# Kernel optimization log

Measured on AMD Instinct MI355X. Metric: run time of the kernel, lower is better.

Reference implementation:

```python
import jax, jax.numpy as jnp
import numpy as np

HIDDEN = 512
N_HEAD = 8
D_HEAD = 64
MAX_REL = 3
B, S = 2, 2048


def setup_inputs() -> dict:
    key = jax.random.key(0)
    ks = jax.random.split(key, 12)
    sc = 1.0 / np.sqrt(HIDDEN)
    return {
        "query": jax.random.normal(ks[0], (B, S, HIDDEN), jnp.float32),
        "key_": jax.random.normal(ks[1], (B, S, HIDDEN), jnp.float32),
        "value": jax.random.normal(ks[2], (B, S, HIDDEN), jnp.float32),
        "mask": jnp.zeros((B, S, S), dtype=bool),
        "pos_matrix": jax.random.randint(ks[3], (S, S), 0, MAX_REL, jnp.int32),
        "Wq": jax.random.normal(ks[4], (HIDDEN, HIDDEN), jnp.float32) * sc,
        "bq": jnp.zeros((HIDDEN,), jnp.float32),
        "Wk": jax.random.normal(ks[5], (HIDDEN, HIDDEN), jnp.float32) * sc,
        "bk": jnp.zeros((HIDDEN,), jnp.float32),
        "Wv": jax.random.normal(ks[6], (HIDDEN, HIDDEN), jnp.float32) * sc,
        "bv": jnp.zeros((HIDDEN,), jnp.float32),
        "Wo": jax.random.normal(ks[7], (HIDDEN, HIDDEN), jnp.float32) * sc,
        "bo": jnp.zeros((HIDDEN,), jnp.float32),
        "rel_table": jax.random.normal(ks[8], (MAX_REL, D_HEAD), jnp.float32) * 0.1,
    }


def reference(query, key_, value, mask, pos_matrix, Wq, bq, Wk, bk, Wv, bv, Wo, bo, rel_table):
    b, s, hid = query.shape
    H, D = N_HEAD, D_HEAD
    q = (query @ Wq + bq).reshape(b, s, H, D)   # [B,S,H,D]
    k = (key_ @ Wk + bk).reshape(b, s, H, D)
    v = (value @ Wv + bv).reshape(b, s, H, D)
    rel = rel_table[pos_matrix[:s, :s]]          # [S,S,D]
    # attn1: content-content; attn2: q vs rel-pos; attn3: k(row) vs rel-pos
    attn1 = jnp.einsum('bihd,bjhd->bhij', q, k)
    attn2 = jnp.einsum('bihd,ijd->bhij', q, rel)
    attn3 = jnp.einsum('bihd,ijd->bhij', k, rel)
    scale = jnp.sqrt(jnp.asarray(D, query.dtype))
    attn = (attn1 + attn2 + attn3) / scale
    attn = jnp.where(mask[:, None, :, :], jnp.asarray(-1e9, attn.dtype), attn)
    attn = jax.nn.softmax(attn, axis=-1)         # dropout=0 (eval)
    x = jnp.einsum('bhij,bjhd->bihd', attn, v).reshape(b, s, hid)
    out = x @ Wo + bo
    return out, attn
```

## Files before the change

kernel.cpp:

```cpp
#include <hip/hip_runtime.h>
#include <math.h>

#define SEQ   2048
#define BATCH 2
#define NHEAD 8
#define HID   512
#define LG8   0.180336880f
#define MASKV -3.0e8f

typedef unsigned char  u8;
typedef unsigned short u16;
typedef short short8 __attribute__((ext_vector_type(8)));
typedef float f32x4  __attribute__((ext_vector_type(4)));

__device__ __forceinline__ u16 f2bf(float f) {
    unsigned u = __float_as_uint(f);
    u = (u + 0x7FFF + ((u >> 16) & 1)) >> 16;
    return (u16)u;
}
__device__ __forceinline__ float bf2f(u16 h) {
    return __uint_as_float(((unsigned)h) << 16);
}

__global__ __launch_bounds__(256) void gemm_bias_kernel(
    const float* __restrict__ A, const float* __restrict__ W,
    const float* __restrict__ bias, float* __restrict__ C, int M)
{
    __shared__ float As[16][68];
    __shared__ float Bs[16][64];
    const int tid = threadIdx.x;
    const int ty = tid >> 4, tx = tid & 15;
    const int row0 = blockIdx.x << 6;
    const int col0 = blockIdx.y << 6;
    const int am = tid >> 2, ak = (tid & 3) << 2;
    const int wk = tid >> 4, wn = (tid & 15) << 2;

    float acc[4][4] = {};
    for (int k0 = 0; k0 < HID; k0 += 16) {
        float4 a4 = *(const float4*)&A[(size_t)(row0 + am) * HID + k0 + ak];
        float4 w4 = *(const float4*)&W[(size_t)(k0 + wk) * HID + col0 + wn];
        __syncthreads();
        As[ak + 0][am] = a4.x; As[ak + 1][am] = a4.y;
        As[ak + 2][am] = a4.z; As[ak + 3][am] = a4.w;
        *(float4*)&Bs[wk][wn] = w4;
        __syncthreads();
        #pragma unroll
        for (int kk = 0; kk < 16; ++kk) {
            float4 a = *(const float4*)&As[kk][ty << 2];
            float4 w = *(const float4*)&Bs[kk][tx << 2];
            acc[0][0] += a.x * w.x; acc[0][1] += a.x * w.y; acc[0][2] += a.x * w.z; acc[0][3] += a.x * w.w;
            acc[1][0] += a.y * w.x; acc[1][1] += a.y * w.y; acc[1][2] += a.y * w.z; acc[1][3] += a.y * w.w;
            acc[2][0] += a.z * w.x; acc[2][1] += a.z * w.y; acc[2][2] += a.z * w.z; acc[2][3] += a.z * w.w;
            acc[3][0] += a.w * w.x; acc[3][1] += a.w * w.y; acc[3][2] += a.w * w.z; acc[3][3] += a.w * w.w;
        }
    }
    float4 bv = *(const float4*)&bias[col0 + (tx << 2)];
    #pragma unroll
    for (int i = 0; i < 4; ++i) {
        float4 o = { acc[i][0] + bv.x, acc[i][1] + bv.y, acc[i][2] + bv.z, acc[i][3] + bv.w };
        *(float4*)&C[(size_t)(row0 + (ty << 2) + i) * HID + col0 + (tx << 2)] = o;
    }
}

__global__ __launch_bounds__(256) void convert_qkv_kernel(
    const float* __restrict__ q, const float* __restrict__ k, const float* __restrict__ v,
    u16* __restrict__ qh, u16* __restrict__ ql,
    u16* __restrict__ kh, u16* __restrict__ kl, u16* __restrict__ vb)
{
    const size_t i = ((size_t)blockIdx.x * 256 + threadIdx.x) * 4;
    float4 qv = *(const float4*)&q[i];
    float4 kv = *(const float4*)&k[i];
    float4 vv = *(const float4*)&v[i];
    ushort4 oqh, oql, okh, okl, ovb;
    float s; u16 hh;
    s = qv.x * LG8; hh = f2bf(s); oqh.x = hh; oql.x = f2bf(s - bf2f(hh));
    s = qv.y * LG8; hh = f2bf(s); oqh.y = hh; oql.y = f2bf(s - bf2f(hh));
    s = qv.z * LG8; hh = f2bf(s); oqh.z = hh; oql.z = f2bf(s - bf2f(hh));
    s = qv.w * LG8; hh = f2bf(s); oqh.w = hh; oql.w = f2bf(s - bf2f(hh));
    s = kv.x;       hh = f2bf(s); okh.x = hh; okl.x = f2bf(s - bf2f(hh));
    s = kv.y;       hh = f2bf(s); okh.y = hh; okl.y = f2bf(s - bf2f(hh));
    s = kv.z;       hh = f2bf(s); okh.z = hh; okl.z = f2bf(s - bf2f(hh));
    s = kv.w;       hh = f2bf(s); okh.w = hh; okl.w = f2bf(s - bf2f(hh));
    ovb.x = f2bf(vv.x); ovb.y = f2bf(vv.y); ovb.z = f2bf(vv.z); ovb.w = f2bf(vv.w);
    *(ushort4*)&qh[i] = oqh; *(ushort4*)&ql[i] = oql;
    *(ushort4*)&kh[i] = okh; *(ushort4*)&kl[i] = okl;
    *(ushort4*)&vb[i] = ovb;
}

__global__ __launch_bounds__(256) void convert_pm_kernel(
    const int* __restrict__ pos, const u8* __restrict__ mask, u8* __restrict__ pm)
{
    const size_t s = ((size_t)blockIdx.x * 256 + threadIdx.x) * 4;
    int4  p = *(const int4*)&pos[s & (size_t)(SEQ * SEQ - 1)];
    uchar4 m = *(const uchar4*)&mask[s];
    uchar4 o;
    o.x = m.x ? (u8)3 : (u8)p.x;
    o.y = m.y ? (u8)3 : (u8)p.y;
    o.z = m.z ? (u8)3 : (u8)p.z;
    o.w = m.w ? (u8)3 : (u8)p.w;
    *(uchar4*)&pm[s] = o;
}

__global__ __launch_bounds__(256) void rel_dots_kernel(
    const float* __restrict__ q, const float* __restrict__ k,
    const float* __restrict__ rel_table, float* __restrict__ dqk)
{
    const int w = blockIdx.x * 4 + (threadIdx.x >> 6);
    const int lane = threadIdx.x & 63;
    const int h = w % NHEAD;
    const int is = w / NHEAD;
    const int b = is / SEQ;
    const int i = is % SEQ;
    const size_t base = (size_t)is * HID + h * 64 + lane;
    const float s = q[base] + k[base];
    float p0 = s * rel_table[lane];
    float p1 = s * rel_table[64 + lane];
    float p2 = s * rel_table[128 + lane];
    #pragma unroll
    for (int off = 32; off; off >>= 1) {
        p0 += __shfl_xor(p0, off);
        p1 += __shfl_xor(p1, off);
        p2 += __shfl_xor(p2, off);
    }
    if (lane == 0) {
        size_t o = (((size_t)b * NHEAD + h) * SEQ + i) << 2;
        dqk[o + 0] = p0 * LG8; dqk[o + 1] = p1 * LG8; dqk[o + 2] = p2 * LG8;
    }
}

__global__ __launch_bounds__(256) void attn_stats_kernel(
    const u16* __restrict__ qh, const u16* __restrict__ ql,
    const u16* __restrict__ kh, const u16* __restrict__ kl,
    const float* __restrict__ dqk, const u8* __restrict__ pm,
    float* __restrict__ invl)
{
    __shared__ __align__(16) u16 Kh[64 * 72];
    __shared__ __align__(16) u16 Kl[64 * 72];
    __shared__ __align__(16) u8  PM[64 * 64];
    __shared__ float Ds[64][4];
    const int tid = threadIdx.x;
    const int wave = tid >> 6, lane = tid & 63;
    const int quad = lane >> 4, l15 = lane & 15;
    const int b = blockIdx.z, h = blockIdx.y, i0 = blockIdx.x << 6;
    const size_t bh = (size_t)(b * NHEAD + h);

    {
        const int i = tid >> 2, r = tid & 3;
        Ds[i][r] = (r == 3) ? MASKV : dqk[((bh * SEQ + i0 + i) << 2) + r];
    }
    const int irow = (wave << 4) + l15;
    const size_t qbase = ((size_t)(b * SEQ + i0 + irow)) * HID + h * 64 + (quad << 3);
    const short8 aqh0 = *(const short8*)&qh[qbase];
    const short8 aqh1 = *(const short8*)&qh[qbase + 32];
    const short8 aql0 = *(const short8*)&ql[qbase];
    const short8 aql1 = *(const short8*)&ql[qbase + 32];

    float srow[4] = {0.f, 0.f, 0.f, 0.f};

    for (int jt = 0; jt < SEQ / 64; ++jt) {
        const int j0 = jt << 6;
        __syncthreads();
        {
            const int rr = tid >> 3, cc = (tid & 7) << 3;
            const size_t g = ((size_t)(b * SEQ + j0 + rr)) * HID + h * 64 + cc;
            *(short8*)&Kh[rr * 72 + cc] = *(const short8*)&kh[g];
            *(short8*)&Kl[rr * 72 + cc] = *(const short8*)&kl[g];
            const size_t g2 = g + (size_t)32 * HID;
            *(short8*)&Kh[(rr + 32) * 72 + cc] = *(const short8*)&kh[g2];
            *(short8*)&Kl[(rr + 32) * 72 + cc] = *(const short8*)&kl[g2];
        }
        {
            const int r = tid >> 2, c = (tid & 3) << 4;
            *(uint4*)&PM[r * 64 + c] =
                *(const uint4*)&pm[((size_t)b * SEQ + i0 + r) * SEQ + j0 + c];
        }
        __syncthreads();

        #pragma unroll
        for (int sub = 0; sub < 4; ++sub) {
            const int n = (sub << 4) + l15;
            const short8 bh0 = *(const short8*)&Kh[n * 72 + (quad << 3)];
            const short8 bh1 = *(const short8*)&Kh[n * 72 + 32 + (quad << 3)];
            const short8 bl0 = *(const short8*)&Kl[n * 72 + (quad << 3)];
            const short8 bl1 = *(const short8*)&Kl[n * 72 + 32 + (quad << 3)];
            f32x4 acc = {0.f, 0.f, 0.f, 0.f};
            acc = __builtin_amdgcn_mfma_f32_16x16x32_bf16(aqh0, bh0, acc, 0, 0, 0);
            acc = __builtin_amdgcn_mfma_f32_16x16x32_bf16(aqh1, bh1, acc, 0, 0, 0);
            acc = __builtin_amdgcn_mfma_f32_16x16x32_bf16(aql0, bh0, acc, 0, 0, 0);
            acc = __builtin_amdgcn_mfma_f32_16x16x32_bf16(aql1, bh1, acc, 0, 0, 0);
            acc = __builtin_amdgcn_mfma_f32_16x16x32_bf16(aqh0, bl0, acc, 0, 0, 0);
            acc = __builtin_amdgcn_mfma_f32_16x16x32_bf16(aqh1, bl1, acc, 0, 0, 0);
            #pragma unroll
            for (int r = 0; r < 4; ++r) {
                const int il = (wave << 4) + (quad << 2) + r;
                const u8 p = PM[il * 64 + (sub << 4) + l15];
                srow[r] += exp2f(acc[r] + Ds[il][p]);
            }
        }
    }
    #pragma unroll
    for (int r = 0; r < 4; ++r) {
        float s = srow[r];
        s += __shfl_xor(s, 1); s += __shfl_xor(s, 2);
        s += __shfl_xor(s, 4); s += __shfl_xor(s, 8);
        if (l15 == 0)
            invl[bh * SEQ + i0 + (wave << 4) + (quad << 2) + r] = 1.0f / s;
    }
}

__global__ __launch_bounds__(256) void attn_fused_kernel(
    const u16* __restrict__ qh, const u16* __restrict__ ql,
    const u16* __restrict__ kh, const u16* __restrict__ kl,
    const u16* __restrict__ vb, const float* __restrict__ dqk,
    const u8* __restrict__ pm, const float* __restrict__ invl,
    float* __restrict__ attn, float* __restrict__ x)
{
    __shared__ __align__(16) u16 Kh[64 * 72];
    __shared__ __align__(16) u16 Kl[64 * 72];
    __shared__ __align__(16) u16 VtT[64 * 72];
    __shared__ __align__(16) u16 Pst[4][16 * 72];
    __shared__ __align__(16) u8  PM[64 * 64];
    __shared__ float Ds[64][4];
    const int tid = threadIdx.x;
    const int wave = tid >> 6, lane = tid & 63;
    const int quad = lane >> 4, l15 = lane & 15;
    const int b = blockIdx.z, h = blockIdx.y, i0 = blockIdx.x << 6;
    const size_t bh = (size_t)(b * NHEAD + h);

    {
        const int i = tid >> 2, r = tid & 3;
        Ds[i][r] = (r == 3) ? MASKV : dqk[((bh * SEQ + i0 + i) << 2) + r];
    }
    float inv_r[4];
    #pragma unroll
    for (int r = 0; r < 4; ++r)
        inv_r[r] = invl[bh * SEQ + i0 + (wave << 4) + (quad << 2) + r];

    const int irow = (wave << 4) + l15;
    const size_t qbase = ((size_t)(b * SEQ + i0 + irow)) * HID + h * 64 + (quad << 3);
    const short8 aqh0 = *(const short8*)&qh[qbase];
    const short8 aqh1 = *(const short8*)&qh[qbase + 32];
    const short8 aql0 = *(const short8*)&ql[qbase];
    const short8 aql1 = *(const short8*)&ql[qbase + 32];

    f32x4 accX[4] = {{0.f,0.f,0.f,0.f},{0.f,0.f,0.f,0.f},{0.f,0.f,0.f,0.f},{0.f,0.f,0.f,0.f}};

    for (int jt = 0; jt < SEQ / 64; ++jt) {
        const int j0 = jt << 6;
        __syncthreads();
        {
            const int rr = tid >> 3, cc = (tid & 7) << 3;
            const size_t g = ((size_t)(b * SEQ + j0 + rr)) * HID + h * 64 + cc;
            *(short8*)&Kh[rr * 72 + cc] = *(const short8*)&kh[g];
            *(short8*)&Kl[rr * 72 + cc] = *(const short8*)&kl[g];
            const size_t g2 = g + (size_t)32 * HID;
            *(short8*)&Kh[(rr + 32) * 72 + cc] = *(const short8*)&kh[g2];
            *(short8*)&Kl[(rr + 32) * 72 + cc] = *(const short8*)&kl[g2];
        }
        {
            const int r = tid >> 2, c = (tid & 3) << 4;
            *(uint4*)&PM[r * 64 + c] =
                *(const uint4*)&pm[((size_t)b * SEQ + i0 + r) * SEQ + j0 + c];
        }
        {
            const int jr = tid & 63, d0 = (tid >> 6) << 4;
            const size_t g = ((size_t)(b * SEQ + j0 + jr)) * HID + h * 64 + d0;
            const short8 v0 = *(const short8*)&vb[g];
            const short8 v1 = *(const short8*)&vb[g + 8];
            #pragma unroll
            for (int e = 0; e < 8; ++e) {
                VtT[(d0 + e) * 72 + jr]     = (u16)v0[e];
                VtT[(d0 + 8 + e) * 72 + jr] = (u16)v1[e];
            }
        }
        __syncthreads();

        #pragma unroll
        for (int sub = 0; sub < 4; ++sub) {
            const int n = (sub << 4) + l15;
            const short8 bh0 = *(const short8*)&Kh[n * 72 + (quad << 3)];
            const short8 bh1 = *(const short8*)&Kh[n * 72 + 32 + (quad << 3)];
            const short8 bl0 = *(const short8*)&Kl[n * 72 + (quad << 3)];
            const short8 bl1 = *(const short8*)&Kl[n * 72 + 32 + (quad << 3)];
            f32x4 acc = {0.f, 0.f, 0.f, 0.f};
            acc = __builtin_amdgcn_mfma_f32_16x16x32_bf16(aqh0, bh0, acc, 0, 0, 0);
            acc = __builtin_amdgcn_mfma_f32_16x16x32_bf16(aqh1, bh1, acc, 0, 0, 0);
            acc = __builtin_amdgcn_mfma_f32_16x16x32_bf16(aql0, bh0, acc, 0, 0, 0);
            acc = __builtin_amdgcn_mfma_f32_16x16x32_bf16(aql1, bh1, acc, 0, 0, 0);
            acc = __builtin_amdgcn_mfma_f32_16x16x32_bf16(aqh0, bl0, acc, 0, 0, 0);
            acc = __builtin_amdgcn_mfma_f32_16x16x32_bf16(aqh1, bl1, acc, 0, 0, 0);
            #pragma unroll
            for (int r = 0; r < 4; ++r) {
                const int il = (wave << 4) + (quad << 2) + r;
                const u8 p = PM[il * 64 + (sub << 4) + l15];
                const float pr = exp2f(acc[r] + Ds[il][p]) * inv_r[r];
                attn[(bh * SEQ + i0 + il) * SEQ + j0 + (sub << 4) + l15] = pr;
                Pst[wave][((quad << 2) + r) * 72 + (sub << 4) + l15] = f2bf(pr);
            }
        }
        const short8 bp0 = *(const short8*)&Pst[wave][l15 * 72 + (quad << 3)];
        const short8 bp1 = *(const short8*)&Pst[wave][l15 * 72 + 32 + (quad << 3)];
        #pragma unroll
        for (int m = 0; m < 4; ++m) {
            const short8 av0 = *(const short8*)&VtT[((m << 4) + l15) * 72 + (quad << 3)];
            const short8 av1 = *(const short8*)&VtT[((m << 4) + l15) * 72 + 32 + (quad << 3)];
            accX[m] = __builtin_amdgcn_mfma_f32_16x16x32_bf16(av0, bp0, accX[m], 0, 0, 0);
            accX[m] = __builtin_amdgcn_mfma_f32_16x16x32_bf16(av1, bp1, accX[m], 0, 0, 0);
        }
    }
    const size_t xrow = ((size_t)(b * SEQ + i0 + (wave << 4) + l15)) * HID + h * 64;
    #pragma unroll
    for (int m = 0; m < 4; ++m) {
        *(f32x4*)&x[xrow + (m << 4) + (quad << 2)] = accX[m];
    }
}

extern "C" void kernel_launch(void* const* d_in, const int* in_sizes, int n_in,
                              void* d_out, int out_size, void* d_ws, size_t ws_size,
                              hipStream_t stream) {
    (void)in_sizes; (void)n_in; (void)out_size; (void)ws_size;
    const float* query = (const float*)d_in[0];
    const float* key_  = (const float*)d_in[1];
    const float* value = (const float*)d_in[2];
    const u8*    mask  = (const u8*)d_in[3];
    const int*   pos   = (const int*)d_in[4];
    const float* Wq = (const float*)d_in[5];
    const float* bq = (const float*)d_in[6];
    const float* Wk = (const float*)d_in[7];
    const float* bk = (const float*)d_in[8];
    const float* Wv = (const float*)d_in[9];
    const float* bv = (const float*)d_in[10];
    const float* Wo = (const float*)d_in[11];
    const float* bo = (const float*)d_in[12];
    const float* rel_table = (const float*)d_in[13];

    float* out  = (float*)d_out;
    float* attn = out + (size_t)BATCH * SEQ * HID;

    float* q_ws = (float*)d_ws;
    float* k_ws = q_ws + (size_t)2097152;
    float* v_ws = k_ws + (size_t)2097152;
    float* dqk  = v_ws + (size_t)2097152;
    float* invl = dqk + (size_t)131072;
    u16* qh = (u16*)(invl + 32768);
    u16* ql = qh + (size_t)2097152;
    u16* kh = ql + (size_t)2097152;
    u16* kl = kh + (size_t)2097152;
    u16* vb = kl + (size_t)2097152;
    u8*  pm = (u8*)(vb + (size_t)2097152);
    float* x_ws = q_ws;

    const dim3 blk(256);
    const int M = BATCH * SEQ;

    gemm_bias_kernel<<<dim3(M / 64, HID / 64), blk, 0, stream>>>(query, Wq, bq, q_ws, M);
    gemm_bias_kernel<<<dim3(M / 64, HID / 64), blk, 0, stream>>>(key_, Wk, bk, k_ws, M);
    gemm_bias_kernel<<<dim3(M / 64, HID / 64), blk, 0, stream>>>(value, Wv, bv, v_ws, M);
    rel_dots_kernel<<<dim3(BATCH * SEQ * NHEAD / 4), blk, 0, stream>>>(q_ws, k_ws, rel_table, dqk);
    convert_qkv_kernel<<<dim3(2048), blk, 0, stream>>>(q_ws, k_ws, v_ws, qh, ql, kh, kl, vb);
    convert_pm_kernel<<<dim3(8192), blk, 0, stream>>>(pos, mask, pm);
    attn_stats_kernel<<<dim3(SEQ / 64, NHEAD, BATCH), blk, 0, stream>>>(
        qh, ql, kh, kl, dqk, pm, invl);
    attn_fused_kernel<<<dim3(SEQ / 64, NHEAD, BATCH), blk, 0, stream>>>(
        qh, ql, kh, kl, vb, dqk, pm, invl, attn, x_ws);
    gemm_bias_kernel<<<dim3(M / 64, HID / 64), blk, 0, stream>>>(x_ws, Wo, bo, out, M);
}
```

Measured before the change: 673.9 us.

## Replace FP32 SIMT projection GEMMs with split-bf16 MFMA GEMMs and fused epilogues

The four linear projections move from scalar FP32 FMA loops to MFMA bf16 matrix instructions using a hi/lo split (three MFMAs per tile) to keep near-FP32 accuracy. Weights are transposed and split by a prep kernel, and activations are split by a convert kernel. The epilogue writes the bf16 hi/lo Q/K/V buffers directly, which removes the separate convert_qkv pass and the FP32 Q/K/V intermediates. In exchange it adds extra small conversion launches per GEMM and drops the low-order a_l*w_l term from each product.

```diff
diff --git a/kernel.cpp b/kernel.cpp
--- a/kernel.cpp
+++ b/kernel.cpp
@@ -22,69 +22,130 @@
     return __uint_as_float(((unsigned)h) << 16);
 }
 
-__global__ __launch_bounds__(256) void gemm_bias_kernel(
-    const float* __restrict__ A, const float* __restrict__ W,
-    const float* __restrict__ bias, float* __restrict__ C, int M)
-{
-    __shared__ float As[16][68];
-    __shared__ float Bs[16][64];
+__global__ __launch_bounds__(256) void prep_w_kernel(
+    const float* __restrict__ W, u16* __restrict__ Wth, u16* __restrict__ Wtl)
+{
+    __shared__ float Ws[64][68];
     const int tid = threadIdx.x;
-    const int ty = tid >> 4, tx = tid & 15;
-    const int row0 = blockIdx.x << 6;
-    const int col0 = blockIdx.y << 6;
-    const int am = tid >> 2, ak = (tid & 3) << 2;
-    const int wk = tid >> 4, wn = (tid & 15) << 2;
-
-    float acc[4][4] = {};
-    for (int k0 = 0; k0 < HID; k0 += 16) {
-        float4 a4 = *(const float4*)&A[(size_t)(row0 + am) * HID + k0 + ak];
-        float4 w4 = *(const float4*)&W[(size_t)(k0 + wk) * HID + col0 + wn];
-        __syncthreads();
-        As[ak + 0][am] = a4.x; As[ak + 1][am] = a4.y;
-        As[ak + 2][am] = a4.z; As[ak + 3][am] = a4.w;
-        *(float4*)&Bs[wk][wn] = w4;
+    const int k0 = blockIdx.x << 6;
+    const int n0 = blockIdx.y << 6;
+    const int rr = tid >> 2, c4 = (tid & 3) << 4;
+    #pragma unroll
+    for (int e = 0; e < 4; ++e) {
+        float4 v = *(const float4*)&W[(size_t)(k0 + rr) * HID + n0 + c4 + (e << 2)];
+        *(float4*)&Ws[rr][c4 + (e << 2)] = v;
+    }
+    __syncthreads();
+    const int nn = tid >> 2, kk = (tid & 3) << 4;
+    u16 hb[16], lb[16];
+    #pragma unroll
+    for (int e = 0; e < 16; ++e) {
+        float x = Ws[kk + e][nn];
+        u16 hi = f2bf(x);
+        hb[e] = hi;
+        lb[e] = f2bf(x - bf2f(hi));
+    }
+    const size_t o = (size_t)(n0 + nn) * HID + k0 + kk;
+    *(short8*)&Wth[o]     = *(short8*)&hb[0];
+    *(short8*)&Wth[o + 8] = *(short8*)&hb[8];
+    *(short8*)&Wtl[o]     = *(short8*)&lb[0];
+    *(short8*)&Wtl[o + 8] = *(short8*)&lb[8];
+}
+
+__global__ __launch_bounds__(256) void convert_split_kernel(
+    const float* __restrict__ src, u16* __restrict__ h, u16* __restrict__ l)
+{
+    const size_t i = ((size_t)blockIdx.x * 256 + threadIdx.x) * 4;
+    float4 v = *(const float4*)&src[i];
+    ushort4 oh, ol; u16 hh;
+    hh = f2bf(v.x); oh.x = hh; ol.x = f2bf(v.x - bf2f(hh));
+    hh = f2bf(v.y); oh.y = hh; ol.y = f2bf(v.y - bf2f(hh));
+    hh = f2bf(v.z); oh.z = hh; ol.z = f2bf(v.z - bf2f(hh));
+    hh = f2bf(v.w); oh.w = hh; ol.w = f2bf(v.w - bf2f(hh));
+    *(ushort4*)&h[i] = oh; *(ushort4*)&l[i] = ol;
+}
+
+template<int MODE>
+__global__ __launch_bounds__(256) void gemm_mfma_kernel(
+    const u16* __restrict__ Ah, const u16* __restrict__ Al,
+    const u16* __restrict__ Wth, const u16* __restrict__ Wtl,
+    const float* __restrict__ bias,
+    float* __restrict__ Cf, u16* __restrict__ Oh, u16* __restrict__ Ol)
+{
+    __shared__ __align__(16) u16 Sa_h[64 * 72];
+    __shared__ __align__(16) u16 Sa_l[64 * 72];
+    __shared__ __align__(16) u16 Sw_h[64 * 72];
+    __shared__ __align__(16) u16 Sw_l[64 * 72];
+    const int tid = threadIdx.x;
+    const int wave = tid >> 6, lane = tid & 63;
+    const int quad = lane >> 4, l15 = lane & 15;
+    const int row0 = blockIdx.x << 6, col0 = blockIdx.y << 6;
+    const int rr = tid >> 2, cc = (tid & 3) << 4;
+
+    const size_t ga = (size_t)(row0 + rr) * HID + cc;
+    const size_t gw = (size_t)(col0 + rr) * HID + cc;
+
+    f32x4 acc[4] = {{0.f,0.f,0.f,0.f},{0.f,0.f,0.f,0.f},{0.f,0.f,0.f,0.f},{0.f,0.f,0.f,0.f}};
+
+    for (int k0 = 0; k0 < HID; k0 += 64) {
+        const short8 ah0 = *(const short8*)&Ah[ga + k0];
+        const short8 ah1 = *(const short8*)&Ah[ga + k0 + 8];
+        const short8 al0 = *(const short8*)&Al[ga + k0];
+        const short8 al1 = *(const short8*)&Al[ga + k0 + 8];
+        const short8 wh0 = *(const short8*)&Wth[gw + k0];
+        const short8 wh1 = *(const short8*)&Wth[gw + k0 + 8];
+        const short8 wl0 = *(const short8*)&Wtl[gw + k0];
+        const short8 wl1 = *(const short8*)&Wtl[gw + k0 + 8];
+        __syncthreads();
+        *(short8*)&Sa_h[rr * 72 + cc]     = ah0;
+        *(short8*)&Sa_h[rr * 72 + cc + 8] = ah1;
+        *(short8*)&Sa_l[rr * 72 + cc]     = al0;
+        *(short8*)&Sa_l[rr * 72 + cc + 8] = al1;
+        *(short8*)&Sw_h[rr * 72 + cc]     = wh0;
+        *(short8*)&Sw_h[rr * 72 + cc + 8] = wh1;
+        *(short8*)&Sw_l[rr * 72 + cc]     = wl0;
+        *(short8*)&Sw_l[rr * 72 + cc + 8] = wl1;
         __syncthreads();
         #pragma unroll
-        for (int kk = 0; kk < 16; ++kk) {
-            float4 a = *(const float4*)&As[kk][ty << 2];
-            float4 w = *(const float4*)&Bs[kk][tx << 2];
-            acc[0][0] += a.x * w.x; acc[0][1] += a.x * w.y; acc[0][2] += a.x * w.z; acc[0][3] += a.x * w.w;
-            acc[1][0] += a.y * w.x; acc[1][1] += a.y * w.y; acc[1][2] += a.y * w.z; acc[1][3] += a.y * w.w;
-            acc[2][0] += a.z * w.x; acc[2][1] += a.z * w.y; acc[2][2] += a.z * w.z; acc[2][3] += a.z * w.w;
-            acc[3][0] += a.w * w.x; acc[3][1] += a.w * w.y; acc[3][2] += a.w * w.z; acc[3][3] += a.w * w.w;
-        }
-    }
-    float4 bv = *(const float4*)&bias[col0 + (tx << 2)];
-    #pragma unroll
-    for (int i = 0; i < 4; ++i) {
-        float4 o = { acc[i][0] + bv.x, acc[i][1] + bv.y, acc[i][2] + bv.z, acc[i][3] + bv.w };
-        *(float4*)&C[(size_t)(row0 + (ty << 2) + i) * HID + col0 + (tx << 2)] = o;
-    }
-}
-
-__global__ __launch_bounds__(256) void convert_qkv_kernel(
-    const float* __restrict__ q, const float* __restrict__ k, const float* __restrict__ v,
-    u16* __restrict__ qh, u16* __restrict__ ql,
-    u16* __restrict__ kh, u16* __restrict__ kl, u16* __restrict__ vb)
-{
-    const size_t i = ((size_t)blockIdx.x * 256 + threadIdx.x) * 4;
-    float4 qv = *(const float4*)&q[i];
-    float4 kv = *(const float4*)&k[i];
-    float4 vv = *(const float4*)&v[i];
-    ushort4 oqh, oql, okh, okl, ovb;
-    float s; u16 hh;
-    s = qv.x * LG8; hh = f2bf(s); oqh.x = hh; oql.x = f2bf(s - bf2f(hh));
-    s = qv.y * LG8; hh = f2bf(s); oqh.y = hh; oql.y = f2bf(s - bf2f(hh));
-    s = qv.z * LG8; hh = f2bf(s); oqh.z = hh; oql.z = f2bf(s - bf2f(hh));
-    s = qv.w * LG8; hh = f2bf(s); oqh.w = hh; oql.w = f2bf(s - bf2f(hh));
-    s = kv.x;       hh = f2bf(s); okh.x = hh; okl.x = f2bf(s - bf2f(hh));
-    s = kv.y;       hh = f2bf(s); okh.y = hh; okl.y = f2bf(s - bf2f(hh));
-    s = kv.z;       hh = f2bf(s); okh.z = hh; okl.z = f2bf(s - bf2f(hh));
-    s = kv.w;       hh = f2bf(s); okh.w = hh; okl.w = f2bf(s - bf2f(hh));
-    ovb.x = f2bf(vv.x); ovb.y = f2bf(vv.y); ovb.z = f2bf(vv.z); ovb.w = f2bf(vv.w);
-    *(ushort4*)&qh[i] = oqh; *(ushort4*)&ql[i] = oql;
-    *(ushort4*)&kh[i] = okh; *(ushort4*)&kl[i] = okl;
-    *(ushort4*)&vb[i] = ovb;
+        for (int s = 0; s < 2; ++s) {
+            const int ao = ((wave << 4) + l15) * 72 + (s << 5) + (quad << 3);
+            const short8 fa_h = *(const short8*)&Sa_h[ao];
+            const short8 fa_l = *(const short8*)&Sa_l[ao];
+            #pragma unroll
+            for (int nt = 0; nt < 4; ++nt) {
+                const int bo = ((nt << 4) + l15) * 72 + (s << 5) + (quad << 3);
+                const short8 fb_h = *(const short8*)&Sw_h[bo];
+                const short8 fb_l = *(const short8*)&Sw_l[bo];
+                acc[nt] = __builtin_amdgcn_mfma_f32_16x16x32_bf16(fa_h, fb_h, acc[nt], 0, 0, 0);
+                acc[nt] = __builtin_amdgcn_mfma_f32_16x16x32_bf16(fa_l, fb_h, acc[nt], 0, 0, 0);
+                acc[nt] = __builtin_amdgcn_mfma_f32_16x16x32_bf16(fa_h, fb_l, acc[nt], 0, 0, 0);
+            }
+        }
+    }
+    #pragma unroll
+    for (int nt = 0; nt < 4; ++nt) {
+        const int col = col0 + (nt << 4) + l15;
+        const float bv = bias[col];
+        #pragma unroll
+        for (int r = 0; r < 4; ++r) {
+            const size_t row = (size_t)(row0 + (wave << 4) + (quad << 2) + r);
+            const float v = acc[nt][r] + bv;
+            if constexpr (MODE == 0) {
+                Cf[row * HID + col] = v;
+            } else if constexpr (MODE == 1) {
+                const float sv = v * LG8;
+                const u16 hi = f2bf(sv);
+                Oh[row * HID + col] = hi;
+                Ol[row * HID + col] = f2bf(sv - bf2f(hi));
+            } else if constexpr (MODE == 2) {
+                const u16 hi = f2bf(v);
+                Oh[row * HID + col] = hi;
+                Ol[row * HID + col] = f2bf(v - bf2f(hi));
+            } else {
+                Oh[row * HID + col] = f2bf(v);
+            }
+        }
+    }
 }
 
 __global__ __launch_bounds__(256) void convert_pm_kernel(
@@ -102,7 +163,8 @@
 }
 
 __global__ __launch_bounds__(256) void rel_dots_kernel(
-    const float* __restrict__ q, const float* __restrict__ k,
+    const u16* __restrict__ qh, const u16* __restrict__ ql,
+    const u16* __restrict__ kh, const u16* __restrict__ kl,
     const float* __restrict__ rel_table, float* __restrict__ dqk)
 {
     const int w = blockIdx.x * 4 + (threadIdx.x >> 6);
@@ -112,7 +174,9 @@
     const int b = is / SEQ;
     const int i = is % SEQ;
     const size_t base = (size_t)is * HID + h * 64 + lane;
-    const float s = q[base] + k[base];
+    const float qs = bf2f(qh[base]) + bf2f(ql[base]);
+    const float kv = bf2f(kh[base]) + bf2f(kl[base]);
+    const float s = qs + LG8 * kv;
     float p0 = s * rel_table[lane];
     float p1 = s * rel_table[64 + lane];
     float p2 = s * rel_table[128 + lane];
@@ -124,7 +188,7 @@
     }
     if (lane == 0) {
         size_t o = (((size_t)b * NHEAD + h) * SEQ + i) << 2;
-        dqk[o + 0] = p0 * LG8; dqk[o + 1] = p1 * LG8; dqk[o + 2] = p2 * LG8;
+        dqk[o + 0] = p0; dqk[o + 1] = p1; dqk[o + 2] = p2;
     }
 }
 
@@ -337,31 +401,47 @@
     float* out  = (float*)d_out;
     float* attn = out + (size_t)BATCH * SEQ * HID;
 
-    float* q_ws = (float*)d_ws;
-    float* k_ws = q_ws + (size_t)2097152;
-    float* v_ws = k_ws + (size_t)2097152;
-    float* dqk  = v_ws + (size_t)2097152;
-    float* invl = dqk + (size_t)131072;
-    u16* qh = (u16*)(invl + 32768);
+    u16* qh = (u16*)d_ws;
     u16* ql = qh + (size_t)2097152;
     u16* kh = ql + (size_t)2097152;
     u16* kl = kh + (size_t)2097152;
     u16* vb = kl + (size_t)2097152;
-    u8*  pm = (u8*)(vb + (size_t)2097152);
-    float* x_ws = q_ws;
+    float* dqk  = (float*)(vb + (size_t)2097152);
+    float* invl = dqk + (size_t)131072;
+    u8*  pm  = (u8*)(invl + (size_t)32768);
+    float* x_ws = (float*)(pm + (size_t)8388608);
+    u16* bufAh = (u16*)(x_ws + (size_t)2097152);
+    u16* bufAl = bufAh + (size_t)2097152;
+    u16* Wth = bufAl + (size_t)2097152;
+    u16* Wtl = Wth + (size_t)262144;
 
     const dim3 blk(256);
-    const int M = BATCH * SEQ;
-
-    gemm_bias_kernel<<<dim3(M / 64, HID / 64), blk, 0, stream>>>(query, Wq, bq, q_ws, M);
-    gemm_bias_kernel<<<dim3(M / 64, HID / 64), blk, 0, stream>>>(key_, Wk, bk, k_ws, M);
-    gemm_bias_kernel<<<dim3(M / 64, HID / 64), blk, 0, stream>>>(value, Wv, bv, v_ws, M);
-    rel_dots_kernel<<<dim3(BATCH * SEQ * NHEAD / 4), blk, 0, stream>>>(q_ws, k_ws, rel_table, dqk);
-    convert_qkv_kernel<<<dim3(2048), blk, 0, stream>>>(q_ws, k_ws, v_ws, qh, ql, kh, kl, vb);
+    const dim3 gemm_grid(64, 8);
+    const dim3 prep_grid(8, 8);
+
+    prep_w_kernel<<<prep_grid, blk, 0, stream>>>(Wq, Wth, Wtl);
+    convert_split_kernel<<<dim3(2048), blk, 0, stream>>>(query, bufAh, bufAl);
+    gemm_mfma_kernel<1><<<gemm_grid, blk, 0, stream>>>(bufAh, bufAl, Wth, Wtl, bq,
+                                                       nullptr, qh, ql);
+    prep_w_kernel<<<prep_grid, blk, 0, stream>>>(Wk, Wth, Wtl);
+    convert_split_kernel<<<dim3(2048), blk, 0, stream>>>(key_, bufAh, bufAl);
+    gemm_mfma_kernel<2><<<gemm_grid, blk, 0, stream>>>(bufAh, bufAl, Wth, Wtl, bk,
+                                                       nullptr, kh, kl);
+    prep_w_kernel<<<prep_grid, blk, 0, stream>>>(Wv, Wth, Wtl);
+    convert_split_kernel<<<dim3(2048), blk, 0, stream>>>(value, bufAh, bufAl);
+    gemm_mfma_kernel<3><<<gemm_grid, blk, 0, stream>>>(bufAh, bufAl, Wth, Wtl, bv,
+                                                       nullptr, vb, nullptr);
+
+    rel_dots_kernel<<<dim3(BATCH * SEQ * NHEAD / 4), blk, 0, stream>>>(
+        qh, ql, kh, kl, rel_table, dqk);
     convert_pm_kernel<<<dim3(8192), blk, 0, stream>>>(pos, mask, pm);
     attn_stats_kernel<<<dim3(SEQ / 64, NHEAD, BATCH), blk, 0, stream>>>(
         qh, ql, kh, kl, dqk, pm, invl);
     attn_fused_kernel<<<dim3(SEQ / 64, NHEAD, BATCH), blk, 0, stream>>>(
         qh, ql, kh, kl, vb, dqk, pm, invl, attn, x_ws);
-    gemm_bias_kernel<<<dim3(M / 64, HID / 64), blk, 0, stream>>>(x_ws, Wo, bo, out, M);
-}
+
+    prep_w_kernel<<<prep_grid, blk, 0, stream>>>(Wo, Wth, Wtl);
+    convert_split_kernel<<<dim3(2048), blk, 0, stream>>>(x_ws, bufAh, bufAl);
+    gemm_mfma_kernel<0><<<gemm_grid, blk, 0, stream>>>(bufAh, bufAl, Wth, Wtl, bo,
+                                                       out, nullptr, nullptr);
+}
```

New measurement: 596.6 us. 1.13x faster.
